# Kernel tuning notes

Hardware: AMD Instinct MI355X
Metric: run time of the kernel (lower is better)

## Reference

```python
import jax, jax.numpy as jnp
import numpy as np

NODE_FEAT = 200  # F.interpolate size in run_all_node
TOPN = 2         # StitchModel.topn


def _node_feats(img, mask, flow, n_inst, max_pix):
    """Vectorized run_all_node: per-instance gather, linear interp to NODE_FEAT,
    3x3 sign histogram of flow[:2], mean of flow[2]. mask holds labels 1..n_inst;
    max_pix is a static upper bound on pixels per instance."""
    flat = mask.reshape(-1) - 1                       # labels 0..N-1
    order = jnp.argsort(flat)                         # stable sort by label
    counts = jax.ops.segment_sum(jnp.ones_like(flat), flat, num_segments=n_inst)
    starts = jnp.concatenate([jnp.zeros((1,), counts.dtype), jnp.cumsum(counts)[:-1]])
    j = jnp.arange(max_pix)
    pos = starts[:, None] + jnp.minimum(j[None, :], counts[:, None] - 1)
    idx = order[pos]                                  # [N, max_pix] padded pixel indices
    valid = j[None, :] < counts[:, None]              # [N, max_pix]
    iv = img.reshape(-1)[idx]                         # instance intensity profiles
    fx = flow[0].reshape(-1)[idx]
    fy = flow[1].reshape(-1)[idx]
    fz = flow[2].reshape(-1)[idx]
    cf = counts.astype(img.dtype)
    zflow = jnp.where(valid, fz, 0).sum(1) / cf       # flows[-1][m].mean()

    def interp(v, L):                                 # torch linear interp, align_corners=False
        Lf = L.astype(img.dtype)
        p = jnp.clip((jnp.arange(NODE_FEAT, dtype=img.dtype) + 0.5) * (Lf / NODE_FEAT) - 0.5,
                     0.0, Lf - 1.0)
        i0 = jnp.floor(p).astype(jnp.int32)
        i1 = jnp.minimum(i0 + 1, L - 1)
        w = p - i0.astype(img.dtype)
        return v[i0] * (1 - w) + v[i1] * w

    nodes = jax.vmap(interp)(iv, counts)              # [N, 200]
    # hist_flow_vector: bins ordered (x:<0,==0,>0) x (y:<0,==0,>0) -> 3*cx+cy
    cx = jnp.where(fx < 0, 0, jnp.where(fx == 0, 1, 2))
    cy = jnp.where(fy < 0, 0, jnp.where(fy == 0, 1, 2))
    bins = cx * 3 + cy
    oh = (bins[..., None] == jnp.arange(9)) & valid[..., None]
    hist = oh.sum(1).astype(img.dtype)                # [N, 9]
    return jnp.concatenate([nodes, hist], -1), zflow


def setup_inputs() -> dict:
    H = W = 2048
    N = 4096
    pix = (H * W) // N
    key = jax.random.key(0)
    ks = jax.random.split(key, 8)

    def make_mask(k):
        labels = (jnp.arange(H * W, dtype=jnp.int32) // pix) + 1   # labels 1..N
        perm = jax.random.permutation(k, H * W)
        return labels[perm].reshape(H, W)

    def make_bbox(k):
        u = jax.random.uniform(k, (N, 4), jnp.float32)
        centers = u[:, :2] * H
        sizes = u[:, 2:] * 49.0 + 1.0                               # nonzero w/h (asserted)
        return jnp.concatenate([centers, sizes], -1)

    return {
        "img1": jax.random.normal(ks[0], (H, W), jnp.float32),
        "img2": jax.random.normal(ks[1], (H, W), jnp.float32),
        "flow1": jax.random.normal(ks[2], (3, H, W), jnp.float32),
        "flow2": jax.random.normal(ks[3], (3, H, W), jnp.float32),
        "bbox1": make_bbox(ks[4]),
        "bbox2": make_bbox(ks[5]),
        "mask1": make_mask(ks[6]),
        "mask2": make_mask(ks[7]),
    }


def reference(img1, img2, flow1, flow2, bbox1, bbox2, mask1, mask2):
    N1, N2 = bbox1.shape[0], bbox2.shape[0]
    max1 = mask1.size // N1   # static bound on pixels/instance (equal-partition masks)
    max2 = mask2.size // N2
    node1, zf1 = _node_feats(img1, mask1, flow1, N1, max1)
    node2, zf2 = _node_feats(img2, mask2, flow2, N2, max2)
    x = jnp.concatenate([node1, node2], 0)            # [(N1+N2), 209]
    # build_one_graph_low_ram: per row, TOPN smallest center distances
    d = jnp.sqrt(((bbox1[:, None, :2] - bbox2[None, :, :2]) ** 2).sum(-1))  # [N1,N2]
    _, nbr = jax.lax.top_k(-d, TOPN)                  # smallest-first, like argsort[:topn]
    src = jnp.repeat(jnp.arange(N1), TOPN)            # [N1*TOPN]
    dst = nbr.reshape(-1)
    edge_index = jnp.stack([src, dst + N1])           # [2, N1*TOPN]
    edge_attr = jnp.stack([
        zf1[src], zf2[dst],
        bbox1[src, 0] - bbox2[dst, 0],
        bbox1[src, 1] - bbox2[dst, 1],
        bbox1[src, 2] / bbox2[dst, 2],
        bbox1[src, 3] / bbox2[dst, 3],
    ], -1)                                            # [N1*TOPN, 6]
    return x, edge_index, edge_attr
```

## Files before the change

kernel.cpp:

```cpp
#include <hip/hip_runtime.h>
#include <math.h>

#pragma clang fp contract(off)

#define HW      (2048*2048)
#define NI      4096
#define MAXPIX  1024
#define NF      200
#define FEAT    209
#define NE      (NI*2)
#define XSIZE   ((2*NI)*FEAT)
#define EIOFF   XSIZE
#define EAOFF   (EIOFF + 2*NE)

#define S       8192
#define CHK     (HW/S)
#define TOTCHK  (2*CHK)
#define NBPI    256
#define LPB     16
#define NBG     (2*NBPI)
#define REC     (2*HW)
#define BTOT    (LPB*MAXPIX)
#define NWS     16
#define NXCD    8

template<int NB>
__device__ __forceinline__ unsigned long long match_bits(int v) {
    unsigned long long m = ~0ull;
    #pragma unroll
    for (int bit = 0; bit < NB; ++bit) {
        unsigned long long bb = __ballot((v >> bit) & 1);
        m &= ((v >> bit) & 1) ? bb : ~bb;
    }
    return m;
}

__global__ void __launch_bounds__(512) count_zf_kernel(const int* __restrict__ mask1,
        const int* __restrict__ mask2, const float* __restrict__ flow1,
        const float* __restrict__ flow2, unsigned* __restrict__ cntA,
        float* __restrict__ zfpart) {
    __shared__ unsigned cnt[8][NBPI];
    __shared__ float zfp[NI];
    int t = threadIdx.x, w = t >> 6, lane = t & 63;
    for (int j = t; j < 8*NBPI; j += 512) ((unsigned*)cnt)[j] = 0u;
    for (int j = t; j < NI; j += 512) zfp[j] = 0.f;
    __syncthreads();
    int c = blockIdx.x;
    int img = c / CHK;
    const int4*   mask  = (const int4*)(img ? mask2 : mask1);
    const float4* flowz = (const float4*)((img ? flow2 : flow1) + 2L*HW);
    long base4 = (long)(c - img*CHK) * (S/4) + (long)w * (S/32);
    #pragma unroll
    for (int it = 0; it < S/32; it += 64) {
        int4   l4 = mask[base4 + it + lane];
        float4 fz = flowz[base4 + it + lane];
        atomicAdd(&cnt[w][(l4.x-1) >> 4], 1u);
        atomicAdd(&cnt[w][(l4.y-1) >> 4], 1u);
        atomicAdd(&cnt[w][(l4.z-1) >> 4], 1u);
        atomicAdd(&cnt[w][(l4.w-1) >> 4], 1u);
        atomicAdd(&zfp[l4.x-1], fz.x);
        atomicAdd(&zfp[l4.y-1], fz.y);
        atomicAdd(&zfp[l4.z-1], fz.z);
        atomicAdd(&zfp[l4.w-1], fz.w);
    }
    __syncthreads();
    if (t < NBPI) {
        unsigned s = 0;
        #pragma unroll
        for (int q = 0; q < 8; ++q) s += cnt[q][t];
        cntA[(long)c * NBPI + t] = s;
    }
    float* zdst = zfpart + (long)c * NI;
    for (int j = t; j < NI; j += 512) zdst[j] = zfp[j];
}

__global__ void __launch_bounds__(1024) scan_zf_kernel(unsigned* __restrict__ cntA,
        const float* __restrict__ zfpart, float* __restrict__ zfm) {
    __shared__ float red[16][64];
    int* wsum = (int*)red;
    int b = blockIdx.x;
    int t = threadIdx.x, lane = t & 63, w = t >> 6;
    if (b < NBG) {
        int img = b >> 8, lb = b & (NBPI - 1);
        unsigned e = 0;
        if (t < CHK) e = cntA[((long)img*CHK + t)*NBPI + lb];
        int incl = (int)e;
        #pragma unroll
        for (int off = 1; off < 64; off <<= 1) {
            int o = __shfl_up(incl, off);
            if (lane >= off) incl += o;
        }
        if (lane == 63) wsum[w] = incl;
        __syncthreads();
        if (t < CHK) {
            int add = 0;
            for (int q = 0; q < w; ++q) add += wsum[q];
            cntA[((long)img*CHK + t)*NBPI + lb] = (unsigned)(incl + add - (int)e);
        }
    } else {
        int b2 = b - NBG;
        int img = b2 >> 6;
        int l0  = (b2 & 63) * 64;
        int rg = t >> 6;
        const float* p = zfpart + ((long)img*CHK + rg)*NI + l0 + lane;
        float s = 0.f;
        #pragma unroll 8
        for (int r = 0; r < CHK; r += 16) s += p[(long)r*NI];
        red[rg][lane] = s;
        __syncthreads();
        if (t < 64) {
            float sum = 0.f;
            #pragma unroll
            for (int g = 0; g < 16; ++g) sum += red[g][t];
            zfm[img*NI + l0 + t] = sum * (1.0f/(float)MAXPIX);
        }
    }
}

__global__ void __launch_bounds__(1024, 8) sort_kernel(
        const float* __restrict__ img1, const float* __restrict__ img2,
        const float* __restrict__ flow1, const float* __restrict__ flow2,
        const int* __restrict__ mask1, const int* __restrict__ mask2,
        const unsigned* __restrict__ cntA,
        float* __restrict__ riv, unsigned char* __restrict__ rmeta) {
    __shared__ float ivs[S];
    __shared__ unsigned short smeta[S];
    __shared__ unsigned short cw[NWS][NBPI];
    int* wsum  = (int*)smeta;
    int* gofsA = (int*)cw;
    int t = threadIdx.x, w = t >> 6, lane = t & 63;
    int bid = blockIdx.x;
    int c = (bid & (NXCD-1)) * (TOTCHK/NXCD) + (bid >> 3);
    int img = c / CHK;
    const int*   mask  = img ? mask2  : mask1;
    const float* image = img ? img2   : img1;
    const float* flow  = img ? flow2  : flow1;
    long base = (long)(c - img*CHK) * S;
    unsigned pre = 0;
    if (t < NBPI) pre = cntA[(long)c * NBPI + t];
    for (int j = t; j < NWS*NBPI; j += 1024) ((unsigned short*)cw)[j] = 0;
    {
        const int4*   mk = (const int4*)mask;
        const float4* iv = (const float4*)image;
        const float4* fx = (const float4*)flow;
        const float4* fy = (const float4*)(flow + HW);
        long i0 = (base >> 2) + (long)w*128 + lane;
        long i1 = i0 + 64;
        int4   m0 = mk[i0], m1 = mk[i1];
        float4 v0 = iv[i0], v1 = iv[i1];
        float4 x0 = fx[i0], x1 = fx[i1];
        float4 y0 = fy[i0], y1 = fy[i1];
        int p0 = (w<<9) + (lane<<2);
        ushort4 s0, s1;
        s0.x = (unsigned short)((m0.x-1) | (((x0.x<0.f?0:(x0.x==0.f?1:2))*3 + (y0.x<0.f?0:(y0.x==0.f?1:2))) << 12));
        s0.y = (unsigned short)((m0.y-1) | (((x0.y<0.f?0:(x0.y==0.f?1:2))*3 + (y0.y<0.f?0:(y0.y==0.f?1:2))) << 12));
        s0.z = (unsigned short)((m0.z-1) | (((x0.z<0.f?0:(x0.z==0.f?1:2))*3 + (y0.z<0.f?0:(y0.z==0.f?1:2))) << 12));
        s0.w = (unsigned short)((m0.w-1) | (((x0.w<0.f?0:(x0.w==0.f?1:2))*3 + (y0.w<0.f?0:(y0.w==0.f?1:2))) << 12));
        s1.x = (unsigned short)((m1.x-1) | (((x1.x<0.f?0:(x1.x==0.f?1:2))*3 + (y1.x<0.f?0:(y1.x==0.f?1:2))) << 12));
        s1.y = (unsigned short)((m1.y-1) | (((x1.y<0.f?0:(x1.y==0.f?1:2))*3 + (y1.y<0.f?0:(y1.y==0.f?1:2))) << 12));
        s1.z = (unsigned short)((m1.z-1) | (((x1.z<0.f?0:(x1.z==0.f?1:2))*3 + (y1.z<0.f?0:(y1.z==0.f?1:2))) << 12));
        s1.w = (unsigned short)((m1.w-1) | (((x1.w<0.f?0:(x1.w==0.f?1:2))*3 + (y1.w<0.f?0:(y1.w==0.f?1:2))) << 12));
        *(float4*)&ivs[p0]         = v0;
        *(float4*)&ivs[p0 + 256]   = v1;
        *(ushort4*)&smeta[p0]       = s0;
        *(ushort4*)&smeta[p0 + 256] = s1;
    }
    __syncthreads();
    int   pk[8];
    float piv[8];
    unsigned long long ltmask = (1ull << lane) - 1ull;
    #pragma unroll
    for (int it = 0; it < 8; ++it) {
        int p = (w<<9) + (it<<6) + lane;
        float ivx = ivs[p];
        int mt = (int)smeta[p];
        int bkt = (mt & 4095) >> 4;
        unsigned long long m = match_bits<8>(bkt);
        int cb = __popcll(m & ltmask);
        int ct = __popcll(m);
        piv[it] = ivx;
        pk[it] = (mt & 0xFFFF) | (cb << 16) | (ct << 22);
        if (cb == 0) cw[w][bkt] += (unsigned short)ct;
    }
    __syncthreads();
    int tot = 0, incl = 0;
    if (t < NBPI) {
        #pragma unroll
        for (int q = 0; q < NWS; ++q) tot += cw[q][t];
        incl = tot;
        #pragma unroll
        for (int off = 1; off < 64; off <<= 1) {
            int o = __shfl_up(incl, off);
            if (lane >= off) incl += o;
        }
        if (lane == 63) wsum[w] = incl;
    }
    __syncthreads();
    int gof = 0;
    if (t < NBPI) {
        int add = 0;
        for (int q = 0; q < w; ++q) add += wsum[q];
        int excl = incl + add - tot;
        int run = excl;
        #pragma unroll
        for (int q = 0; q < NWS; ++q) {
            int cq = cw[q][t];
            cw[q][t] = (unsigned short)run;
            run += cq;
        }
        gof = (img*NBPI + t) * BTOT + (int)pre - excl;
    }
    __syncthreads();
    #pragma unroll
    for (int it = 0; it < 8; ++it) {
        int pkv = pk[it];
        int l = pkv & 4095, bin = (pkv >> 12) & 15;
        int cb = (pkv >> 16) & 63, ct = (pkv >> 22) & 127;
        int bkt = l >> 4;
        int r0 = (int)cw[w][bkt];
        int dst = r0 + cb;
        if (cb == ct - 1) cw[w][bkt] = (unsigned short)(r0 + ct);
        ivs[dst] = piv[it];
        smeta[dst] = (unsigned short)((bkt << 8) | (bin << 4) | (l & 15));
    }
    __syncthreads();
    if (t < NBPI) gofsA[t] = gof;
    __syncthreads();
    for (int j = t; j < S; j += 1024) {
        int ms = (int)smeta[j];
        int b = ms >> 8;
        int g = gofsA[b] + j;
        riv[g]   = ivs[j];
        rmeta[g] = (unsigned char)(ms & 0xFF);
    }
}

__global__ void __launch_bounds__(1024) stageB_kernel(
        const float* __restrict__ riv, const unsigned char* __restrict__ rmeta,
        float* __restrict__ out) {
    __shared__ float acc[LPB * NF];
    __shared__ float s_tw[MAXPIX];
    __shared__ int   s_tk[MAXPIX];
    __shared__ int   hist[LPB * 9];
    __shared__ int   qc[16][LPB];
    __shared__ int   cur[16][LPB];
    int t = threadIdx.x, w = t >> 6, lane = t & 63;
    int gb = blockIdx.x;
    for (int j = t; j < LPB*NF; j += 1024) acc[j] = 0.f;
    if (t < MAXPIX) s_tk[t] = -1;
    if (t < LPB*9) hist[t] = 0;
    for (int j = t; j < 16*LPB; j += 1024) ((int*)qc)[j] = 0;
    __syncthreads();
    if (t < NF) {
        const float Lf = (float)MAXPIX;
        float p = ((float)t + 0.5f) * (Lf / (float)NF) - 0.5f;
        p = fminf(fmaxf(p, 0.0f), Lf - 1.0f);
        int i0 = (int)floorf(p);
        int i1 = min(i0 + 1, MAXPIX - 1);
        float wg = p - (float)i0;
        s_tk[i0] = t; s_tw[i0] = 1.0f - wg;
        s_tk[i1] = t; s_tw[i1] = wg;
    }
    long base = (long)gb * BTOT;
    const int qsz = BTOT / 16;
    int qbeg = w * qsz;
    const int nit = qsz / 64;
    unsigned long long ltmask = (1ull << lane) - 1ull;
    {
        const uchar4* rm4 = (const uchar4*)(rmeta + base + qbeg);
        #pragma unroll
        for (int it = 0; it < nit/4; ++it) {
            uchar4 m = rm4[it*64 + lane];
            atomicAdd(&qc[w][m.x & 15], 1);
            atomicAdd(&qc[w][m.y & 15], 1);
            atomicAdd(&qc[w][m.z & 15], 1);
            atomicAdd(&qc[w][m.w & 15], 1);
        }
    }
    __syncthreads();
    if (t < LPB) {
        int s = 0;
        #pragma unroll
        for (int q = 0; q < 16; ++q) { cur[q][t] = s; s += qc[q][t]; }
    }
    __syncthreads();
    #pragma unroll 4
    for (int it = 0; it < nit; ++it) {
        int i = qbeg + it*64 + lane;
        int meta = (int)rmeta[base + i];
        float iv = riv[base + i];
        int ll = meta & 15;
        unsigned long long m = match_bits<4>(ll);
        int cb = __popcll(m & ltmask);
        int ct = __popcll(m);
        int r0 = cur[w][ll];
        int rank = r0 + cb;
        if (cb == ct - 1) cur[w][ll] = r0 + ct;
        atomicAdd(&hist[ll*9 + (meta >> 4)], 1);
        int k = s_tk[rank];
        if (k >= 0) atomicAdd(&acc[ll*NF + k], iv * s_tw[rank]);
    }
    __syncthreads();
    for (int j = t; j < LPB*FEAT; j += 1024) {
        int r = j / FEAT, k = j - r*FEAT;
        float v = (k < NF) ? acc[r*NF + k] : (float)hist[r*9 + (k - NF)];
        out[(long)gb * LPB * FEAT + j] = v;
    }
}

__device__ __forceinline__ bool better(float d, int j, float d2, int j2) {
    return d < d2 || (d == d2 && j < j2);
}

__global__ void __launch_bounds__(256) edge_kernel(const float* __restrict__ bbox1,
                                                   const float* __restrict__ bbox2,
                                                   const float* __restrict__ zfm,
                                                   float* __restrict__ out) {
    __shared__ float sbx[NI], sby[NI];
    int wave = threadIdx.x >> 6, lane = threadIdx.x & 63;
    for (int r = threadIdx.x; r < NI; r += 256) {
        float4 b = ((const float4*)bbox2)[r];
        sbx[r] = b.x; sby[r] = b.y;
    }
    __syncthreads();
    int i = blockIdx.x * 4 + wave;
    float c1x = bbox1[i*4 + 0], c1y = bbox1[i*4 + 1];
    float d0 = INFINITY; int j0 = 0x7fffffff;
    float d1 = INFINITY; int j1 = 0x7fffffff;
    for (int t = 0; t < NI; t += 64) {
        int j = t + lane;
        float dx = c1x - sbx[j];
        float dy = c1y - sby[j];
        float dsq = dx*dx + dy*dy;
        float d = (float)sqrt((double)dsq);
        if (better(d, j, d0, j0)) { d1 = d0; j1 = j0; d0 = d; j0 = j; }
        else if (better(d, j, d1, j1)) { d1 = d; j1 = j; }
    }
    for (int off = 32; off; off >>= 1) {
        float od0 = __shfl_down(d0, off); int oj0 = __shfl_down(j0, off);
        float od1 = __shfl_down(d1, off); int oj1 = __shfl_down(j1, off);
        if (better(od0, oj0, d0, j0)) {
            if (better(d0, j0, od1, oj1)) { d1 = d0; j1 = j0; }
            else                          { d1 = od1; j1 = oj1; }
            d0 = od0; j0 = oj0;
        } else if (better(od0, oj0, d1, j1)) { d1 = od0; j1 = oj0; }
    }
    if (lane == 0) {
        float z1 = zfm[i];
        int js[2] = { j0, j1 };
        for (int t = 0; t < 2; ++t) {
            int e = i*2 + t, j = js[t];
            out[EIOFF + e]      = (float)i;
            out[EIOFF + NE + e] = (float)(j + NI);
            float* ea = out + EAOFF + (long)e * 6;
            ea[0] = z1;
            ea[1] = zfm[NI + j];
            ea[2] = c1x - bbox2[j*4 + 0];
            ea[3] = c1y - bbox2[j*4 + 1];
            ea[4] = bbox1[i*4 + 2] / bbox2[j*4 + 2];
            ea[5] = bbox1[i*4 + 3] / bbox2[j*4 + 3];
        }
    }
}

extern "C" void kernel_launch(void* const* d_in, const int* in_sizes, int n_in,
                              void* d_out, int out_size, void* d_ws, size_t ws_size,
                              hipStream_t stream) {
    const float* img1  = (const float*)d_in[0];
    const float* img2  = (const float*)d_in[1];
    const float* flow1 = (const float*)d_in[2];
    const float* flow2 = (const float*)d_in[3];
    const float* bbox1 = (const float*)d_in[4];
    const float* bbox2 = (const float*)d_in[5];
    const int*   mask1 = (const int*)d_in[6];
    const int*   mask2 = (const int*)d_in[7];
    float* out = (float*)d_out;

    char* ws = (char*)d_ws;
    size_t off = 0;
    unsigned* cntA   = (unsigned*)(ws + off); off += (size_t)TOTCHK * NBPI * 4;
    float*    riv    = (float*)(ws + off);    off += (size_t)REC * 4;
    float*    zfpart = (float*)(ws + off);    off += (size_t)TOTCHK * NI * 4;
    float*    zfm    = (float*)(ws + off);    off += 2 * NI * 4;
    unsigned char* rmeta = (unsigned char*)(ws + off); off += (size_t)REC;

    hipLaunchKernelGGL(count_zf_kernel, dim3(TOTCHK), dim3(512), 0, stream,
                       mask1, mask2, flow1, flow2, cntA, zfpart);
    hipLaunchKernelGGL(scan_zf_kernel, dim3(NBG + 128), dim3(1024), 0, stream,
                       cntA, zfpart, zfm);
    hipLaunchKernelGGL(sort_kernel, dim3(TOTCHK), dim3(1024), 0, stream,
                       img1, img2, flow1, flow2, mask1, mask2, cntA, riv, rmeta);
    hipLaunchKernelGGL(stageB_kernel, dim3(NBG), dim3(1024), 0, stream,
                       riv, rmeta, out);
    hipLaunchKernelGGL(edge_kernel, dim3(NI/4), dim3(256), 0, stream,
                       bbox1, bbox2, zfm, out);
}
```

Before: 302.6 us.

## Move zflow reduction into stageB and aggregate shared atomics with wave ballots

The zflow partial-sum reduction moves out of the scan kernel and runs as 128 extra blocks of stageB, so the scan kernel becomes a small 512-thread prefix scan on the critical path before the sort. In stageB, the per-wave label counting and the histogram updates now use match/ballot masks so that one leader lane per group does a single shared-memory add in place of one atomic per lane. The per-lane label match is rebuilt from individual ballots over the meta bits, which adds ballot instructions to each iteration in exchange for fewer contended LDS atomics.

```diff
diff --git a/kernel.cpp b/kernel.cpp
--- a/kernel.cpp
+++ b/kernel.cpp
@@ -74,47 +74,23 @@
     for (int j = t; j < NI; j += 512) zdst[j] = zfp[j];
 }
 
-__global__ void __launch_bounds__(1024) scan_zf_kernel(unsigned* __restrict__ cntA,
-        const float* __restrict__ zfpart, float* __restrict__ zfm) {
-    __shared__ float red[16][64];
-    int* wsum = (int*)red;
+__global__ void __launch_bounds__(512) scan_kernel(unsigned* __restrict__ cntA) {
+    __shared__ int wsum[8];
     int b = blockIdx.x;
+    int img = b >> 8, lb = b & (NBPI - 1);
     int t = threadIdx.x, lane = t & 63, w = t >> 6;
-    if (b < NBG) {
-        int img = b >> 8, lb = b & (NBPI - 1);
-        unsigned e = 0;
-        if (t < CHK) e = cntA[((long)img*CHK + t)*NBPI + lb];
-        int incl = (int)e;
-        #pragma unroll
-        for (int off = 1; off < 64; off <<= 1) {
-            int o = __shfl_up(incl, off);
-            if (lane >= off) incl += o;
-        }
-        if (lane == 63) wsum[w] = incl;
-        __syncthreads();
-        if (t < CHK) {
-            int add = 0;
-            for (int q = 0; q < w; ++q) add += wsum[q];
-            cntA[((long)img*CHK + t)*NBPI + lb] = (unsigned)(incl + add - (int)e);
-        }
-    } else {
-        int b2 = b - NBG;
-        int img = b2 >> 6;
-        int l0  = (b2 & 63) * 64;
-        int rg = t >> 6;
-        const float* p = zfpart + ((long)img*CHK + rg)*NI + l0 + lane;
-        float s = 0.f;
-        #pragma unroll 8
-        for (int r = 0; r < CHK; r += 16) s += p[(long)r*NI];
-        red[rg][lane] = s;
-        __syncthreads();
-        if (t < 64) {
-            float sum = 0.f;
-            #pragma unroll
-            for (int g = 0; g < 16; ++g) sum += red[g][t];
-            zfm[img*NI + l0 + t] = sum * (1.0f/(float)MAXPIX);
-        }
-    }
+    unsigned e = cntA[((long)img*CHK + t)*NBPI + lb];
+    int incl = (int)e;
+    #pragma unroll
+    for (int off = 1; off < 64; off <<= 1) {
+        int o = __shfl_up(incl, off);
+        if (lane >= off) incl += o;
+    }
+    if (lane == 63) wsum[w] = incl;
+    __syncthreads();
+    int add = 0;
+    for (int q = 0; q < w; ++q) add += wsum[q];
+    cntA[((long)img*CHK + t)*NBPI + lb] = (unsigned)(incl + add - (int)e);
 }
 
 __global__ void __launch_bounds__(1024, 8) sort_kernel(
@@ -237,19 +213,39 @@
 
 __global__ void __launch_bounds__(1024) stageB_kernel(
         const float* __restrict__ riv, const unsigned char* __restrict__ rmeta,
-        float* __restrict__ out) {
+        const float* __restrict__ zfpart, float* __restrict__ out,
+        float* __restrict__ zfm) {
     __shared__ float acc[LPB * NF];
     __shared__ float s_tw[MAXPIX];
     __shared__ int   s_tk[MAXPIX];
     __shared__ int   hist[LPB * 9];
     __shared__ int   qc[16][LPB];
     __shared__ int   cur[16][LPB];
+    __shared__ float red[16][64];
     int t = threadIdx.x, w = t >> 6, lane = t & 63;
-    int gb = blockIdx.x;
+    int b = blockIdx.x;
+    if (b >= NBG) {
+        int b2 = b - NBG;
+        int img = b2 >> 6;
+        int l0  = (b2 & 63) * 64;
+        const float* p = zfpart + ((long)img*CHK + w)*NI + l0 + lane;
+        float s = 0.f;
+        #pragma unroll 8
+        for (int r = 0; r < CHK; r += 16) s += p[(long)r*NI];
+        red[w][lane] = s;
+        __syncthreads();
+        if (t < 64) {
+            float sum = 0.f;
+            #pragma unroll
+            for (int g = 0; g < 16; ++g) sum += red[g][t];
+            zfm[img*NI + l0 + t] = sum * (1.0f/(float)MAXPIX);
+        }
+        return;
+    }
     for (int j = t; j < LPB*NF; j += 1024) acc[j] = 0.f;
     if (t < MAXPIX) s_tk[t] = -1;
     if (t < LPB*9) hist[t] = 0;
-    for (int j = t; j < 16*LPB; j += 1024) ((int*)qc)[j] = 0;
+    if (t < 16*LPB) ((int*)qc)[t] = 0;
     __syncthreads();
     if (t < NF) {
         const float Lf = (float)MAXPIX;
@@ -261,20 +257,21 @@
         s_tk[i0] = t; s_tw[i0] = 1.0f - wg;
         s_tk[i1] = t; s_tw[i1] = wg;
     }
-    long base = (long)gb * BTOT;
+    long base = (long)b * BTOT;
     const int qsz = BTOT / 16;
     int qbeg = w * qsz;
-    const int nit = qsz / 64;
     unsigned long long ltmask = (1ull << lane) - 1ull;
     {
         const uchar4* rm4 = (const uchar4*)(rmeta + base + qbeg);
         #pragma unroll
-        for (int it = 0; it < nit/4; ++it) {
+        for (int it = 0; it < 4; ++it) {
             uchar4 m = rm4[it*64 + lane];
-            atomicAdd(&qc[w][m.x & 15], 1);
-            atomicAdd(&qc[w][m.y & 15], 1);
-            atomicAdd(&qc[w][m.z & 15], 1);
-            atomicAdd(&qc[w][m.w & 15], 1);
+            int l0 = m.x & 15, l1 = m.y & 15, l2 = m.z & 15, l3 = m.w & 15;
+            unsigned long long mm;
+            mm = match_bits<4>(l0); if ((mm & ltmask) == 0) qc[w][l0] += __popcll(mm);
+            mm = match_bits<4>(l1); if ((mm & ltmask) == 0) qc[w][l1] += __popcll(mm);
+            mm = match_bits<4>(l2); if ((mm & ltmask) == 0) qc[w][l2] += __popcll(mm);
+            mm = match_bits<4>(l3); if ((mm & ltmask) == 0) qc[w][l3] += __popcll(mm);
         }
     }
     __syncthreads();
@@ -284,19 +281,31 @@
         for (int q = 0; q < 16; ++q) { cur[q][t] = s; s += qc[q][t]; }
     }
     __syncthreads();
-    #pragma unroll 4
-    for (int it = 0; it < nit; ++it) {
+    #pragma unroll
+    for (int it = 0; it < 16; ++it) {
         int i = qbeg + it*64 + lane;
         int meta = (int)rmeta[base + i];
         float iv = riv[base + i];
         int ll = meta & 15;
-        unsigned long long m = match_bits<4>(ll);
-        int cb = __popcll(m & ltmask);
-        int ct = __popcll(m);
+        unsigned long long mll = ~0ull, m8;
+        #pragma unroll
+        for (int bit = 0; bit < 4; ++bit) {
+            unsigned long long bb = __ballot((meta >> bit) & 1);
+            mll &= ((meta >> bit) & 1) ? bb : ~bb;
+        }
+        m8 = mll;
+        #pragma unroll
+        for (int bit = 4; bit < 8; ++bit) {
+            unsigned long long bb = __ballot((meta >> bit) & 1);
+            m8 &= ((meta >> bit) & 1) ? bb : ~bb;
+        }
+        int cb = __popcll(mll & ltmask);
+        int ct = __popcll(mll);
         int r0 = cur[w][ll];
         int rank = r0 + cb;
         if (cb == ct - 1) cur[w][ll] = r0 + ct;
-        atomicAdd(&hist[ll*9 + (meta >> 4)], 1);
+        if ((m8 & ltmask) == 0)
+            atomicAdd(&hist[ll*9 + (meta >> 4)], __popcll(m8));
         int k = s_tk[rank];
         if (k >= 0) atomicAdd(&acc[ll*NF + k], iv * s_tw[rank]);
     }
@@ -304,7 +313,7 @@
     for (int j = t; j < LPB*FEAT; j += 1024) {
         int r = j / FEAT, k = j - r*FEAT;
         float v = (k < NF) ? acc[r*NF + k] : (float)hist[r*9 + (k - NF)];
-        out[(long)gb * LPB * FEAT + j] = v;
+        out[(long)b * LPB * FEAT + j] = v;
     }
 }
 
@@ -386,12 +395,11 @@
 
     hipLaunchKernelGGL(count_zf_kernel, dim3(TOTCHK), dim3(512), 0, stream,
                        mask1, mask2, flow1, flow2, cntA, zfpart);
-    hipLaunchKernelGGL(scan_zf_kernel, dim3(NBG + 128), dim3(1024), 0, stream,
-                       cntA, zfpart, zfm);
+    hipLaunchKernelGGL(scan_kernel, dim3(NBG), dim3(512), 0, stream, cntA);
     hipLaunchKernelGGL(sort_kernel, dim3(TOTCHK), dim3(1024), 0, stream,
                        img1, img2, flow1, flow2, mask1, mask2, cntA, riv, rmeta);
-    hipLaunchKernelGGL(stageB_kernel, dim3(NBG), dim3(1024), 0, stream,
-                       riv, rmeta, out);
+    hipLaunchKernelGGL(stageB_kernel, dim3(NBG + 128), dim3(1024), 0, stream,
+                       riv, rmeta, zfpart, out, zfm);
     hipLaunchKernelGGL(edge_kernel, dim3(NI/4), dim3(256), 0, stream,
                        bbox1, bbox2, zfm, out);
 }
```

Measured after the change: 299.2 us. Within noise of the previous version (-1.1%).
